# Optimization experiments

Hardware: AMD Instinct MI355X
Metric: run time of the kernel (lower is better)

The kernel has to match this reference:

```python
import jax, jax.numpy as jnp
import numpy as np

N_CAP = 10000   # self.n default: >= bs so the [:, :n] slice is a no-op
MARGIN = 0.3    # forward default m


def setup_inputs() -> dict:
    key = jax.random.key(0)
    k1, k2 = jax.random.split(key)
    bs, dim = 2048, 256
    sketch = jax.random.normal(k1, (bs, dim), dtype=jnp.float32)
    photo = jax.random.normal(k2, (bs, dim), dtype=jnp.float32)
    return {"sketch": sketch, "photo": photo}


def reference(sketch, photo):
    # d == 2 branch: Euclidean distances.
    bs = sketch.shape[0]
    # positive distance per row: ||sketch_i - photo_i||_2  -> (bs,)
    pos = jnp.sqrt(jnp.sum((sketch - photo) ** 2, axis=1))
    # negative distance matrix neg[i, j] = ||sketch_j - photo_i||_2  -> (bs, bs)
    # GEMM identity instead of materializing the (bs,bs,dim) broadcast:
    # ||a-b||^2 = ||a||^2 + ||b||^2 - 2 a.b  (same math, fused/efficient form)
    sn = jnp.sum(sketch ** 2, axis=1)            # (bs,)
    pn = jnp.sum(photo ** 2, axis=1)             # (bs,)
    cross = jnp.einsum('id,jd->ij', photo, sketch)  # (bs, bs): photo rows x sketch cols
    neg2 = jnp.maximum(pn[:, None] + sn[None, :] - 2.0 * cross, 0.0)
    neg = jnp.sqrt(neg2)
    # triplet: pos broadcasts as a row vector (pos[j] - neg[i,j]) + m
    tl = pos[None, :] - neg + MARGIN
    # zero the diagonal, relu, column-cap, then mean over dim 1 and overall
    eye = jnp.eye(bs, dtype=tl.dtype)
    tl = jax.nn.relu(tl * (1.0 - eye))
    tl = tl[:, :N_CAP]
    return jnp.mean(jnp.mean(tl, axis=1))
```

## Files before the change

### kernel.cpp

```cpp
#include <hip/hip_runtime.h>

#define BS 2048
#define DIM 256
#define MARGIN_F 0.3f

typedef __attribute__((ext_vector_type(4))) float f32x4;
typedef __attribute__((ext_vector_type(2))) __fp16 fp16x2;
typedef __attribute__((ext_vector_type(8))) _Float16 f16x8;

__device__ __forceinline__ void gload_lds16(const void* g, void* l) {
    __builtin_amdgcn_global_load_lds((const __attribute__((address_space(1))) void*)g,
                                     (__attribute__((address_space(3))) void*)l,
                                     16, 0, 0);
}

__global__ __launch_bounds__(256) void tl_prep(const float* __restrict__ sketch,
                                               const float* __restrict__ photo,
                                               float* __restrict__ sn,
                                               float* __restrict__ pn,
                                               float* __restrict__ pos,
                                               _Float16* __restrict__ hs,
                                               _Float16* __restrict__ hp) {
    const int t = threadIdx.x;
    const int w = t >> 6, lane = t & 63;
    const int row = blockIdx.x * 4 + w;
    const float4 s4 = *reinterpret_cast<const float4*>(&sketch[(size_t)row * DIM + lane * 4]);
    const float4 p4 = *reinterpret_cast<const float4*>(&photo [(size_t)row * DIM + lane * 4]);

    float vs = s4.x * s4.x + s4.y * s4.y + s4.z * s4.z + s4.w * s4.w;
    float vp = p4.x * p4.x + p4.y * p4.y + p4.z * p4.z + p4.w * p4.w;
    float dx = s4.x - p4.x, dy = s4.y - p4.y, dz = s4.z - p4.z, dw = s4.w - p4.w;
    float vd = dx * dx + dy * dy + dz * dz + dw * dw;
    #pragma unroll
    for (int off = 32; off > 0; off >>= 1) {
        vs += __shfl_down(vs, off);
        vp += __shfl_down(vp, off);
        vd += __shfl_down(vd, off);
    }
    if (lane == 0) { sn[row] = vs; pn[row] = vp; pos[row] = sqrtf(vd); }

    union { fp16x2 h2[2]; uint2 u; } cs, cp;
    cs.h2[0] = __builtin_amdgcn_cvt_pkrtz(s4.x, s4.y);
    cs.h2[1] = __builtin_amdgcn_cvt_pkrtz(s4.z, s4.w);
    cp.h2[0] = __builtin_amdgcn_cvt_pkrtz(p4.x, p4.y);
    cp.h2[1] = __builtin_amdgcn_cvt_pkrtz(p4.z, p4.w);
    const int qg = lane >> 1;
    const int pg = (qg & 24) | ((qg & 7) ^ (row & 7));
    const size_t dsth = (size_t)row * DIM + pg * 8 + (lane & 1) * 4;
    *reinterpret_cast<uint2*>(&hs[dsth]) = cs.u;
    *reinterpret_cast<uint2*>(&hp[dsth]) = cp.u;
}

__global__ __launch_bounds__(256) void tl_gemm(const _Float16* __restrict__ hp,
                                               const _Float16* __restrict__ hs,
                                               const float* __restrict__ sn,
                                               const float* __restrict__ pn,
                                               const float* __restrict__ pos,
                                               float* __restrict__ partials) {
    __shared__ _Float16 As[4][64][64];
    __shared__ _Float16 Bs[4][64][64];

    const int b = blockIdx.x;
    const int xcd = b & 7, slot = b >> 3;
    const int by = (xcd & 3) * 8 + (slot >> 4);
    const int bx = (xcd >> 2) * 16 + (slot & 15);

    const int t = threadIdx.x;
    const int i0 = by * 64;
    const int j0 = bx * 64;
    const int w = t >> 6, lane = t & 63;
    const int wr = (w >> 1) * 32;
    const int wc = (w & 1) * 32;
    const int r16 = lane & 15, g = lane >> 4;

    f32x4 acc00 = {}, acc01 = {}, acc10 = {}, acc11 = {};

    const int srow = w * 16 + (lane >> 3);
    const int sch  = lane & 7;
    const _Float16* gA0 = &hp[(size_t)(i0 + srow) * DIM + sch * 8];
    const _Float16* gB0 = &hs[(size_t)(j0 + srow) * DIM + sch * 8];

    #pragma unroll
    for (int kw = 0; kw < 4; ++kw) {
        const int koff = kw * 64;
        gload_lds16(gA0 + koff,           &As[kw][w * 16][0]);
        gload_lds16(gA0 + 8 * DIM + koff, &As[kw][w * 16 + 8][0]);
        gload_lds16(gB0 + koff,           &Bs[kw][w * 16][0]);
        gload_lds16(gB0 + 8 * DIM + koff, &Bs[kw][w * 16 + 8][0]);
    }
    __syncthreads();

    const int xa = r16 & 7;
    #pragma unroll
    for (int kw = 0; kw < 4; ++kw) {
        #pragma unroll
        for (int ks = 0; ks < 2; ++ks) {
            const int q8 = ((ks * 4 + g) ^ xa) * 8;
            f16x8 a0 = *reinterpret_cast<const f16x8*>(&As[kw][wr + r16][q8]);
            f16x8 a1 = *reinterpret_cast<const f16x8*>(&As[kw][wr + 16 + r16][q8]);
            f16x8 b0 = *reinterpret_cast<const f16x8*>(&Bs[kw][wc + r16][q8]);
            f16x8 b1 = *reinterpret_cast<const f16x8*>(&Bs[kw][wc + 16 + r16][q8]);
            acc00 = __builtin_amdgcn_mfma_f32_16x16x32_f16(a0, b0, acc00, 0, 0, 0);
            acc01 = __builtin_amdgcn_mfma_f32_16x16x32_f16(a0, b1, acc01, 0, 0, 0);
            acc10 = __builtin_amdgcn_mfma_f32_16x16x32_f16(a1, b0, acc10, 0, 0, 0);
            acc11 = __builtin_amdgcn_mfma_f32_16x16x32_f16(a1, b1, acc11, 0, 0, 0);
        }
    }

    const int jl = r16;
    const int rl = g * 4;
    float partial = 0.0f;

    #pragma unroll
    for (int n = 0; n < 2; ++n) {
        const int j = j0 + wc + n * 16 + jl;
        const float snj = sn[j];
        const float posj = pos[j];
        const f32x4 cn0 = (n == 0) ? acc00 : acc01;
        const f32x4 cn1 = (n == 0) ? acc10 : acc11;
        #pragma unroll
        for (int m = 0; m < 2; ++m) {
            const int ibase = i0 + wr + m * 16 + rl;
            const f32x4 cv = (m == 0) ? cn0 : cn1;
            #pragma unroll
            for (int r = 0; r < 4; ++r) {
                const int i = ibase + r;
                const float c = cv[r];
                float neg2 = fmaxf(pn[i] + snj - 2.0f * c, 0.0f);
                float tl = posj - sqrtf(neg2) + MARGIN_F;
                partial += (i != j) ? fmaxf(tl, 0.0f) : 0.0f;
            }
        }
    }

    #pragma unroll
    for (int off = 32; off > 0; off >>= 1) partial += __shfl_down(partial, off);
    __shared__ float lsum[4];
    if (lane == 0) lsum[w] = partial;
    __syncthreads();
    if (t == 0)
        partials[b] = lsum[0] + lsum[1] + lsum[2] + lsum[3];
}

__global__ __launch_bounds__(256) void tl_reduce(const float* __restrict__ partials,
                                                 float* __restrict__ out) {
    const int t = threadIdx.x;
    const float4 v = reinterpret_cast<const float4*>(partials)[t];
    float s = v.x + v.y + v.z + v.w;
    #pragma unroll
    for (int off = 32; off > 0; off >>= 1) s += __shfl_down(s, off);
    __shared__ float lsum[4];
    const int w = t >> 6, lane = t & 63;
    if (lane == 0) lsum[w] = s;
    __syncthreads();
    if (t == 0)
        out[0] = (lsum[0] + lsum[1] + lsum[2] + lsum[3]) * (1.0f / ((float)BS * (float)BS));
}

extern "C" void kernel_launch(void* const* d_in, const int* in_sizes, int n_in,
                              void* d_out, int out_size, void* d_ws, size_t ws_size,
                              hipStream_t stream) {
    const float* sketch = (const float*)d_in[0];
    const float* photo  = (const float*)d_in[1];
    float* out = (float*)d_out;

    float* sn  = (float*)d_ws;
    float* pn  = sn + BS;
    float* pos = pn + BS;
    _Float16* hp = (_Float16*)(pos + BS);
    _Float16* hs = hp + (size_t)BS * DIM;
    float* partials = (float*)(hs + (size_t)BS * DIM);

    tl_prep<<<dim3(BS / 4), dim3(256), 0, stream>>>(sketch, photo, sn, pn, pos, hs, hp);

    tl_gemm<<<dim3(1024), dim3(256), 0, stream>>>(hp, hs, sn, pn, pos, partials);

    tl_reduce<<<dim3(1), dim3(256), 0, stream>>>(partials, out);
}
```

Baseline: 19.60 us.

## Process two column tiles per GEMM block, reusing the loaded A tile

Each GEMM block now loads its 64-row photo tile once and loops over two adjacent 64-column sketch tiles, computing and reducing a partial sum for each. The grid shrinks from 1024 to 512 blocks on a plain 2D layout, dropping the XCD-aware block swizzle. The aim is to halve redundant A-tile global loads and per-block launch overhead. In exchange the second B-tile load is not overlapped with compute, extra barriers are added, parallelism is halved, and L2 locality from the old XCD mapping may be lost.

```diff
diff --git a/kernel.cpp b/kernel.cpp
--- a/kernel.cpp
+++ b/kernel.cpp
@@ -59,87 +59,88 @@
                                                float* __restrict__ partials) {
     __shared__ _Float16 As[4][64][64];
     __shared__ _Float16 Bs[4][64][64];
-
-    const int b = blockIdx.x;
-    const int xcd = b & 7, slot = b >> 3;
-    const int by = (xcd & 3) * 8 + (slot >> 4);
-    const int bx = (xcd >> 2) * 16 + (slot & 15);
+    __shared__ float lsum[4];
 
     const int t = threadIdx.x;
+    const int by = blockIdx.y;
+    const int bxh = blockIdx.x;
     const int i0 = by * 64;
-    const int j0 = bx * 64;
     const int w = t >> 6, lane = t & 63;
     const int wr = (w >> 1) * 32;
     const int wc = (w & 1) * 32;
     const int r16 = lane & 15, g = lane >> 4;
 
-    f32x4 acc00 = {}, acc01 = {}, acc10 = {}, acc11 = {};
-
     const int srow = w * 16 + (lane >> 3);
     const int sch  = lane & 7;
     const _Float16* gA0 = &hp[(size_t)(i0 + srow) * DIM + sch * 8];
-    const _Float16* gB0 = &hs[(size_t)(j0 + srow) * DIM + sch * 8];
 
     #pragma unroll
     for (int kw = 0; kw < 4; ++kw) {
-        const int koff = kw * 64;
-        gload_lds16(gA0 + koff,           &As[kw][w * 16][0]);
-        gload_lds16(gA0 + 8 * DIM + koff, &As[kw][w * 16 + 8][0]);
-        gload_lds16(gB0 + koff,           &Bs[kw][w * 16][0]);
-        gload_lds16(gB0 + 8 * DIM + koff, &Bs[kw][w * 16 + 8][0]);
+        gload_lds16(gA0 + kw * 64,           &As[kw][w * 16][0]);
+        gload_lds16(gA0 + 8 * DIM + kw * 64, &As[kw][w * 16 + 8][0]);
     }
-    __syncthreads();
 
     const int xa = r16 & 7;
-    #pragma unroll
-    for (int kw = 0; kw < 4; ++kw) {
-        #pragma unroll
-        for (int ks = 0; ks < 2; ++ks) {
-            const int q8 = ((ks * 4 + g) ^ xa) * 8;
-            f16x8 a0 = *reinterpret_cast<const f16x8*>(&As[kw][wr + r16][q8]);
-            f16x8 a1 = *reinterpret_cast<const f16x8*>(&As[kw][wr + 16 + r16][q8]);
-            f16x8 b0 = *reinterpret_cast<const f16x8*>(&Bs[kw][wc + r16][q8]);
-            f16x8 b1 = *reinterpret_cast<const f16x8*>(&Bs[kw][wc + 16 + r16][q8]);
-            acc00 = __builtin_amdgcn_mfma_f32_16x16x32_f16(a0, b0, acc00, 0, 0, 0);
-            acc01 = __builtin_amdgcn_mfma_f32_16x16x32_f16(a0, b1, acc01, 0, 0, 0);
-            acc10 = __builtin_amdgcn_mfma_f32_16x16x32_f16(a1, b0, acc10, 0, 0, 0);
-            acc11 = __builtin_amdgcn_mfma_f32_16x16x32_f16(a1, b1, acc11, 0, 0, 0);
-        }
-    }
-
-    const int jl = r16;
-    const int rl = g * 4;
-    float partial = 0.0f;
 
     #pragma unroll
-    for (int n = 0; n < 2; ++n) {
-        const int j = j0 + wc + n * 16 + jl;
-        const float snj = sn[j];
-        const float posj = pos[j];
-        const f32x4 cn0 = (n == 0) ? acc00 : acc01;
-        const f32x4 cn1 = (n == 0) ? acc10 : acc11;
+    for (int h = 0; h < 2; ++h) {
+        const int j0 = (bxh * 2 + h) * 64;
+        const _Float16* gB0 = &hs[(size_t)(j0 + srow) * DIM + sch * 8];
         #pragma unroll
-        for (int m = 0; m < 2; ++m) {
-            const int ibase = i0 + wr + m * 16 + rl;
-            const f32x4 cv = (m == 0) ? cn0 : cn1;
+        for (int kw = 0; kw < 4; ++kw) {
+            gload_lds16(gB0 + kw * 64,           &Bs[kw][w * 16][0]);
+            gload_lds16(gB0 + 8 * DIM + kw * 64, &Bs[kw][w * 16 + 8][0]);
+        }
+        __syncthreads();
+
+        f32x4 acc00 = {}, acc01 = {}, acc10 = {}, acc11 = {};
+        #pragma unroll
+        for (int kw = 0; kw < 4; ++kw) {
             #pragma unroll
-            for (int r = 0; r < 4; ++r) {
-                const int i = ibase + r;
-                const float c = cv[r];
-                float neg2 = fmaxf(pn[i] + snj - 2.0f * c, 0.0f);
-                float tl = posj - sqrtf(neg2) + MARGIN_F;
-                partial += (i != j) ? fmaxf(tl, 0.0f) : 0.0f;
+            for (int ks = 0; ks < 2; ++ks) {
+                const int q8 = ((ks * 4 + g) ^ xa) * 8;
+                f16x8 a0 = *reinterpret_cast<const f16x8*>(&As[kw][wr + r16][q8]);
+                f16x8 a1 = *reinterpret_cast<const f16x8*>(&As[kw][wr + 16 + r16][q8]);
+                f16x8 b0 = *reinterpret_cast<const f16x8*>(&Bs[kw][wc + r16][q8]);
+                f16x8 b1 = *reinterpret_cast<const f16x8*>(&Bs[kw][wc + 16 + r16][q8]);
+                acc00 = __builtin_amdgcn_mfma_f32_16x16x32_f16(a0, b0, acc00, 0, 0, 0);
+                acc01 = __builtin_amdgcn_mfma_f32_16x16x32_f16(a0, b1, acc01, 0, 0, 0);
+                acc10 = __builtin_amdgcn_mfma_f32_16x16x32_f16(a1, b0, acc10, 0, 0, 0);
+                acc11 = __builtin_amdgcn_mfma_f32_16x16x32_f16(a1, b1, acc11, 0, 0, 0);
             }
         }
+
+        const int jl = r16, rl = g * 4;
+        float partial = 0.0f;
+        #pragma unroll
+        for (int n = 0; n < 2; ++n) {
+            const int j = j0 + wc + n * 16 + jl;
+            const float snj = sn[j];
+            const float posj = pos[j];
+            const f32x4 cn0 = (n == 0) ? acc00 : acc01;
+            const f32x4 cn1 = (n == 0) ? acc10 : acc11;
+            #pragma unroll
+            for (int m = 0; m < 2; ++m) {
+                const int ibase = i0 + wr + m * 16 + rl;
+                const f32x4 cv = (m == 0) ? cn0 : cn1;
+                #pragma unroll
+                for (int r = 0; r < 4; ++r) {
+                    const int i = ibase + r;
+                    float neg2 = fmaxf(pn[i] + snj - 2.0f * cv[r], 0.0f);
+                    float tl = posj - sqrtf(neg2) + MARGIN_F;
+                    partial += (i != j) ? fmaxf(tl, 0.0f) : 0.0f;
+                }
+            }
+        }
+
+        #pragma unroll
+        for (int off = 32; off > 0; off >>= 1) partial += __shfl_down(partial, off);
+        if (lane == 0) lsum[w] = partial;
+        __syncthreads();
+        if (t == 0)
+            partials[by * 32 + bxh * 2 + h] = lsum[0] + lsum[1] + lsum[2] + lsum[3];
+        __syncthreads();
     }
-
-    #pragma unroll
-    for (int off = 32; off > 0; off >>= 1) partial += __shfl_down(partial, off);
-    __shared__ float lsum[4];
-    if (lane == 0) lsum[w] = partial;
-    __syncthreads();
-    if (t == 0)
-        partials[b] = lsum[0] + lsum[1] + lsum[2] + lsum[3];
 }
 
 __global__ __launch_bounds__(256) void tl_reduce(const float* __restrict__ partials,
@@ -173,7 +174,8 @@
 
     tl_prep<<<dim3(BS / 4), dim3(256), 0, stream>>>(sketch, photo, sn, pn, pos, hs, hp);
 
-    tl_gemm<<<dim3(1024), dim3(256), 0, stream>>>(hp, hs, sn, pn, pos, partials);
+    dim3 grid(16, 32);
+    tl_gemm<<<grid, dim3(256), 0, stream>>>(hp, hs, sn, pn, pos, partials);
 
     tl_reduce<<<dim3(1), dim3(256), 0, stream>>>(partials, out);
 }
```

New measurement: 19.35 us. No clear change (-1.3%).
